# Kernel tuning notes

Hardware: AMD Instinct MI355X
Metric: run time of the kernel (lower is better)

## Reference

```python
import jax, jax.numpy as jnp
import numpy as np

IN_F = 4096
OUT_F = 4096
NNZ = 167772  # int(IN_F*OUT_F*0.01)
B, S = 4, 2048
ALPHA = 1.0  # self.alpha (privacy enabled)


def setup_inputs() -> dict:
    key = jax.random.key(0)
    k1, k2, k3, k4, k5 = jax.random.split(key, 5)
    x = jax.random.normal(k1, (B, S, IN_F), dtype=jnp.float32)
    # quantized-then-dequantized base weights stored in fp16
    base_weights = (jax.random.normal(k2, (OUT_F, IN_F), dtype=jnp.float32) * 0.02).astype(jnp.float16)
    # sparse outlier residual in COO form (equivalent to the module's CSR buffers)
    ortho_rows = jax.random.randint(k3, (NNZ,), 0, OUT_F, dtype=jnp.int32)
    ortho_cols = jax.random.randint(k4, (NNZ,), 0, IN_F, dtype=jnp.int32)
    ortho_vals = (jax.random.normal(k5, (NNZ,), dtype=jnp.float32) * 1e-3).astype(jnp.float16)
    return {"x": x, "base_weights": base_weights, "ortho_vals": ortho_vals,
            "ortho_rows": ortho_rows, "ortho_cols": ortho_cols}


def reference(x, base_weights, ortho_vals, ortho_rows, ortho_cols):
    orig_shape = x.shape
    orig_dtype = x.dtype
    x_flat = x.reshape(-1, IN_F)                                   # [N, in]
    # Base stream: fp16 GEMM, accumulated to fp32 (matches torch.mm on fp16 then .to(f32))
    out_base = jnp.matmul(x_flat.astype(jnp.float16), base_weights.T).astype(jnp.float32)  # [N, out]
    # Ortho stream: sparse CSR residual, computed in fp32 (vals upcast like the module)
    # Scatter the nnz outliers into a dense [out, in] matrix once, then a single GEMM
    # (same math as torch.sparse.mm over the CSR tensor, without per-chunk loops).
    w_ortho = jnp.zeros((OUT_F, IN_F), jnp.float32).at[ortho_rows, ortho_cols].add(
        ortho_vals.astype(jnp.float32))
    out_ortho = jnp.matmul(x_flat.astype(jnp.float32), w_ortho.T)  # [N, out]
    out_flat = out_base + ALPHA * out_ortho
    return out_flat.reshape(orig_shape[:-1] + (OUT_F,)).astype(orig_dtype)
```

## Files before the change

kernel.cpp:

```cpp
#include <hip/hip_runtime.h>
#include <stdint.h>

#define IN_F 4096
#define OUT_F 4096
#define NTOK 8192
#define NNZ_CNT 167772

typedef __attribute__((ext_vector_type(4))) float f32x4;
typedef __attribute__((ext_vector_type(8))) __bf16 bf16x8;
typedef __attribute__((ext_vector_type(8))) unsigned short u16x8;

__device__ __forceinline__ unsigned short f2bf(float f) {
  union { float f; unsigned int i; } u; u.f = f;
  unsigned int i = u.i;
  unsigned int r = (i + 0x7FFFu + ((i >> 16) & 1u)) >> 16;
  return (unsigned short)r;
}
__device__ __forceinline__ float bf2f(unsigned short h) {
  union { unsigned int i; float f; } u; u.i = ((unsigned int)h) << 16;
  return u.f;
}
__device__ __forceinline__ float sanitize(float f, float lim) {
  if (f >= -lim && f <= lim) return f;
  if (f > lim) return lim;
  if (f < -lim) return -lim;
  return 0.f;
}

__global__ void detect_dtype_kernel(const unsigned short* __restrict__ w, int* __restrict__ flag) {
  __shared__ int cnt;
  if (threadIdx.x == 0) cnt = 0;
  __syncthreads();
  int local = 0;
  for (int j = 0; j < 16; ++j) {
    unsigned short u = w[threadIdx.x * 16 + j];
    int e = (u >> 7) & 0xFF;
    if (u != 0 && e >= 107 && e <= 126) local++;
  }
  atomicAdd(&cnt, local);
  __syncthreads();
  if (threadIdx.x == 0) *flag = (cnt >= 3481) ? 0 : 1;
}

__global__ void prep_kernel(const float4* __restrict__ x, u16x8* __restrict__ xb, int n8x,
                            const void* __restrict__ bw, u16x8* __restrict__ wc, int n8w,
                            const int* __restrict__ flag) {
  const bool isf32 = (*flag != 0);
  const int stride = gridDim.x * blockDim.x;
  const int i0 = blockIdx.x * blockDim.x + threadIdx.x;
  for (int i = i0; i < n8x; i += stride) {
    float4 v0 = x[i * 2], v1 = x[i * 2 + 1];
    u16x8 o;
    o[0] = f2bf(sanitize(v0.x, 64.f)); o[1] = f2bf(sanitize(v0.y, 64.f));
    o[2] = f2bf(sanitize(v0.z, 64.f)); o[3] = f2bf(sanitize(v0.w, 64.f));
    o[4] = f2bf(sanitize(v1.x, 64.f)); o[5] = f2bf(sanitize(v1.y, 64.f));
    o[6] = f2bf(sanitize(v1.z, 64.f)); o[7] = f2bf(sanitize(v1.w, 64.f));
    xb[i] = o;
  }
  for (int i = i0; i < n8w; i += stride) {
    u16x8 o;
    if (isf32) {
      const float4* s = (const float4*)bw + i * 2;
      float4 v0 = s[0], v1 = s[1];
      o[0] = f2bf(sanitize(v0.x, 1.f)); o[1] = f2bf(sanitize(v0.y, 1.f));
      o[2] = f2bf(sanitize(v0.z, 1.f)); o[3] = f2bf(sanitize(v0.w, 1.f));
      o[4] = f2bf(sanitize(v1.x, 1.f)); o[5] = f2bf(sanitize(v1.y, 1.f));
      o[6] = f2bf(sanitize(v1.z, 1.f)); o[7] = f2bf(sanitize(v1.w, 1.f));
    } else {
      u16x8 v = ((const u16x8*)bw)[i];
#pragma unroll
      for (int j = 0; j < 8; ++j) o[j] = f2bf(sanitize(bf2f(v[j]), 1.f));
    }
    wc[i] = o;
  }
}

__global__ void scatter_kernel(const void* __restrict__ vals,
                               const int* __restrict__ rows,
                               const int* __restrict__ cols,
                               unsigned short* __restrict__ W,
                               const int* __restrict__ flag) {
  int i = blockIdx.x * blockDim.x + threadIdx.x;
  if (i >= NNZ_CNT) return;
  int r = rows[i], c = cols[i];
  if ((unsigned)r >= OUT_F || (unsigned)c >= IN_F) return;
  float v = (*flag != 0) ? ((const float*)vals)[i] : bf2f(((const unsigned short*)vals)[i]);
  v = sanitize(v, 1.f);
  unsigned int* addr = (unsigned int*)(W + (size_t)r * IN_F + (c & ~1));
  bool hi = (c & 1);
  unsigned int old = *addr, assumed;
  do {
    assumed = old;
    unsigned short h = hi ? (unsigned short)(assumed >> 16) : (unsigned short)(assumed & 0xFFFFu);
    unsigned short nh = f2bf(bf2f(h) + v);
    unsigned int nw = hi ? ((assumed & 0x0000FFFFu) | ((unsigned int)nh << 16))
                         : ((assumed & 0xFFFF0000u) | (unsigned int)nh);
    old = atomicCAS(addr, assumed, nw);
  } while (old != assumed);
}

#define GLOAD16(g, l)                                                                  \
  __builtin_amdgcn_global_load_lds((const __attribute__((address_space(1))) void*)(g), \
                                   (__attribute__((address_space(3))) void*)(l), 16, 0, 0)

__global__ __launch_bounds__(512, 2) void gemm256_kernel(
    const unsigned short* __restrict__ Abf,
    const unsigned short* __restrict__ Bw,
    float* __restrict__ C) {
  __shared__ __align__(16) char lds[131072];
  const int t = threadIdx.x;
  const int l = t & 63;
  const int wv = t >> 6;
  const int wm = wv >> 2;
  const int wn = wv & 3;
  const int l15 = l & 15;

  const int swz = (blockIdx.x & 7) * 64 + (blockIdx.x >> 3);
  const int bm = (swz >> 4) * 256;
  const int bn = (swz & 15) * 256;

  const int srow = t >> 2;
  const int sunit = (t & 3) ^ ((t >> 3) & 3);
  const unsigned short* aS0 = Abf + (size_t)(bm + srow) * IN_F + sunit * 8;
  const unsigned short* aS1 = aS0 + (size_t)128 * IN_F;
  const unsigned short* bS0 = Bw + (size_t)(bn + srow) * IN_F + sunit * 8;
  const unsigned short* bS1 = bS0 + (size_t)128 * IN_F;
  char* dstA = (char*)lds + wv * 1024;
  char* dstB = (char*)lds + 32768 + wv * 1024;

  const int u = (l >> 4) ^ ((l15 >> 1) & 3);
  const int iA = (wm * 128 + l15) * 4 + u;
  const int iB = 2048 + (wn * 64 + l15) * 4 + u;
  const bf16x8* smp = (const bf16x8*)lds;

  f32x4 acc[8][4] = {};

  GLOAD16(aS0 + 0, dstA + 0);          GLOAD16(aS1 + 0, dstA + 8192);
  GLOAD16(bS0 + 0, dstB + 0);          GLOAD16(bS1 + 0, dstB + 8192);
  GLOAD16(aS0 + 32, dstA + 16384);     GLOAD16(aS1 + 32, dstA + 16384 + 8192);
  GLOAD16(bS0 + 32, dstB + 16384);     GLOAD16(bS1 + 32, dstB + 16384 + 8192);
  GLOAD16(aS0 + 64, dstA + 65536);     GLOAD16(aS1 + 64, dstA + 65536 + 8192);
  GLOAD16(bS0 + 64, dstB + 65536);     GLOAD16(bS1 + 64, dstB + 65536 + 8192);
  asm volatile("s_waitcnt vmcnt(8)" ::: "memory");
  asm volatile("s_barrier" ::: "memory");

  for (int kt = 0; kt < 64; ++kt) {
    const int c = kt & 1;
    const int cU = c << 12;
    const int s1 = ((kt + 1 < 64) ? (kt + 1) : 63) * 64 + 32;
    const int s2 = ((kt + 2 < 64) ? (kt + 2) : 63) * 64;
    const int d1 = (c ^ 1) * 65536 + 16384;
    const int d2 = c * 65536;
    bf16x8 av[4], bv[4];

#pragma unroll
    for (int mi = 0; mi < 4; ++mi) av[mi] = smp[cU + iA + mi * 64];
#pragma unroll
    for (int ni = 0; ni < 4; ++ni) bv[ni] = smp[cU + iB + ni * 64];
    GLOAD16(aS0 + s1, dstA + d1);
    GLOAD16(aS1 + s1, dstA + d1 + 8192);
    asm volatile("s_barrier" ::: "memory");
    asm volatile("s_waitcnt lgkmcnt(0)" ::: "memory");
    __builtin_amdgcn_s_setprio(1);
#pragma unroll
    for (int mi = 0; mi < 4; ++mi)
#pragma unroll
      for (int ni = 0; ni < 4; ++ni)
        acc[mi][ni] = __builtin_amdgcn_mfma_f32_16x16x32_bf16(av[mi], bv[ni], acc[mi][ni], 0, 0, 0);
    __builtin_amdgcn_s_setprio(0);
    asm volatile("s_barrier" ::: "memory");

#pragma unroll
    for (int mi = 0; mi < 4; ++mi) av[mi] = smp[cU + iA + (mi + 4) * 64];
    GLOAD16(bS0 + s1, dstB + d1);
    GLOAD16(bS1 + s1, dstB + d1 + 8192);
    asm volatile("s_barrier" ::: "memory");
    asm volatile("s_waitcnt lgkmcnt(0)" ::: "memory");
    __builtin_amdgcn_s_setprio(1);
#pragma unroll
    for (int mi = 0; mi < 4; ++mi)
#pragma unroll
      for (int ni = 0; ni < 4; ++ni)
        acc[mi + 4][ni] = __builtin_amdgcn_mfma_f32_16x16x32_bf16(av[mi], bv[ni], acc[mi + 4][ni], 0, 0, 0);
    __builtin_amdgcn_s_setprio(0);
    asm volatile("s_waitcnt vmcnt(8)" ::: "memory");
    asm volatile("s_barrier" ::: "memory");

#pragma unroll
    for (int mi = 0; mi < 4; ++mi) av[mi] = smp[cU + 1024 + iA + mi * 64];
#pragma unroll
    for (int ni = 0; ni < 4; ++ni) bv[ni] = smp[cU + 1024 + iB + ni * 64];
    GLOAD16(aS0 + s2, dstA + d2);
    GLOAD16(aS1 + s2, dstA + d2 + 8192);
    asm volatile("s_barrier" ::: "memory");
    asm volatile("s_waitcnt lgkmcnt(0)" ::: "memory");
    __builtin_amdgcn_s_setprio(1);
#pragma unroll
    for (int mi = 0; mi < 4; ++mi)
#pragma unroll
      for (int ni = 0; ni < 4; ++ni)
        acc[mi][ni] = __builtin_amdgcn_mfma_f32_16x16x32_bf16(av[mi], bv[ni], acc[mi][ni], 0, 0, 0);
    __builtin_amdgcn_s_setprio(0);
    asm volatile("s_barrier" ::: "memory");

#pragma unroll
    for (int mi = 0; mi < 4; ++mi) av[mi] = smp[cU + 1024 + iA + (mi + 4) * 64];
    GLOAD16(bS0 + s2, dstB + d2);
    GLOAD16(bS1 + s2, dstB + d2 + 8192);
    asm volatile("s_barrier" ::: "memory");
    asm volatile("s_waitcnt lgkmcnt(0)" ::: "memory");
    __builtin_amdgcn_s_setprio(1);
#pragma unroll
    for (int mi = 0; mi < 4; ++mi)
#pragma unroll
      for (int ni = 0; ni < 4; ++ni)
        acc[mi + 4][ni] = __builtin_amdgcn_mfma_f32_16x16x32_bf16(av[mi], bv[ni], acc[mi + 4][ni], 0, 0, 0);
    __builtin_amdgcn_s_setprio(0);
    asm volatile("s_waitcnt vmcnt(8)" ::: "memory");
    asm volatile("s_barrier" ::: "memory");
  }

#pragma unroll
  for (int mi = 0; mi < 8; ++mi) {
#pragma unroll
    for (int ni = 0; ni < 4; ++ni) {
      int row0 = bm + wm * 128 + mi * 16 + ((l >> 4) << 2);
      int col = bn + wn * 64 + ni * 16 + l15;
#pragma unroll
      for (int r = 0; r < 4; ++r)
        C[(size_t)(row0 + r) * OUT_F + col] = acc[mi][ni][r];
    }
  }
}

__global__ __launch_bounds__(256, 3) void gemm_kernel(
    const float* __restrict__ Af, const unsigned short* __restrict__ Bw, float* __restrict__ C) {
  __shared__ bf16x8 smem[2048];
  const int tid = threadIdx.x;
  const int lane = tid & 63;
  const int wv = tid >> 6;
  const int bm = blockIdx.x * 128;
  const int bn = blockIdx.y * 128;
  const int srow = wv * 8 + (lane >> 3);
  const int scol = (lane & 7) * 8;
  const int wr = wv >> 1, wc = wv & 1;
  f32x4 acc[4][4] = {};
  const float* afp[4];
  const unsigned short* bptr[4];
#pragma unroll
  for (int q = 0; q < 4; ++q) {
    afp[q] = Af + (size_t)(bm + q * 32 + srow) * IN_F + scol;
    bptr[q] = Bw + (size_t)(bn + q * 32 + srow) * IN_F + scol;
  }
  char* smbase = (char*)smem;
  for (int k0 = 0; k0 < IN_F; k0 += 64) {
    __syncthreads();
#pragma unroll
    for (int q = 0; q < 4; ++q)
      GLOAD16(bptr[q] + k0, smbase + 16384 + q * 4096 + wv * 1024);
#pragma unroll
    for (int q = 0; q < 4; ++q) {
      const float* s = afp[q] + k0;
      float4 v0 = ((const float4*)s)[0];
      float4 v1 = ((const float4*)s)[1];
      u16x8 p;
      p[0] = f2bf(sanitize(v0.x, 64.f)); p[1] = f2bf(sanitize(v0.y, 64.f));
      p[2] = f2bf(sanitize(v0.z, 64.f)); p[3] = f2bf(sanitize(v0.w, 64.f));
      p[4] = f2bf(sanitize(v1.x, 64.f)); p[5] = f2bf(sanitize(v1.y, 64.f));
      p[6] = f2bf(sanitize(v1.z, 64.f)); p[7] = f2bf(sanitize(v1.w, 64.f));
      ((u16x8*)smem)[q * 256 + wv * 64 + lane] = p;
    }
    __syncthreads();
#pragma unroll
    for (int kk = 0; kk < 2; ++kk) {
      bf16x8 av[4], bv[4];
#pragma unroll
      for (int m = 0; m < 4; ++m)
        av[m] = smem[(wr * 64 + m * 16 + (lane & 15)) * 8 + kk * 4 + (lane >> 4)];
#pragma unroll
      for (int n = 0; n < 4; ++n)
        bv[n] = smem[1024 + (wc * 64 + n * 16 + (lane & 15)) * 8 + kk * 4 + (lane >> 4)];
#pragma unroll
      for (int m = 0; m < 4; ++m)
#pragma unroll
        for (int n = 0; n < 4; ++n)
          acc[m][n] = __builtin_amdgcn_mfma_f32_16x16x32_bf16(av[m], bv[n], acc[m][n], 0, 0, 0);
    }
  }
#pragma unroll
  for (int m = 0; m < 4; ++m)
#pragma unroll
    for (int n = 0; n < 4; ++n) {
      int row0 = bm + wr * 64 + m * 16 + ((lane >> 4) << 2);
      int col = bn + wc * 64 + n * 16 + (lane & 15);
#pragma unroll
      for (int r = 0; r < 4; ++r)
        C[(size_t)(row0 + r) * OUT_F + col] = acc[m][n][r];
    }
}

__global__ void naive_gemm_kernel(const float* __restrict__ x, const void* __restrict__ W,
                                  float* __restrict__ out, const int* __restrict__ flag) {
  const bool isf32 = (*flag != 0);
  int o = blockIdx.x * 256 + threadIdx.x;
  int t = blockIdx.y;
  const float* xr = x + (size_t)t * IN_F;
  float acc = 0.f;
  if (isf32) {
    const float* wr = (const float*)W + (size_t)o * IN_F;
    for (int k = 0; k < IN_F; ++k) acc += bf2f(f2bf(xr[k])) * bf2f(f2bf(sanitize(wr[k], 1.f)));
  } else {
    const unsigned short* wr = (const unsigned short*)W + (size_t)o * IN_F;
    for (int k = 0; k < IN_F; ++k) acc += bf2f(f2bf(xr[k])) * sanitize(bf2f(wr[k]), 1.f);
  }
  out[(size_t)t * OUT_F + o] = acc;
}
__global__ void naive_sparse_kernel(const float* __restrict__ x, const void* __restrict__ vals,
                                    const int* __restrict__ rows, const int* __restrict__ cols,
                                    float* __restrict__ out, const int* __restrict__ flag) {
  const bool isf32 = (*flag != 0);
  int t = blockIdx.x * 256 + threadIdx.x;
  if (t >= NTOK) return;
  const float* xr = x + (size_t)t * IN_F;
  float* orow = out + (size_t)t * OUT_F;
  for (int i = 0; i < NNZ_CNT; ++i) {
    int r = rows[i], c = cols[i];
    if ((unsigned)r >= OUT_F || (unsigned)c >= IN_F) continue;
    float v = isf32 ? ((const float*)vals)[i] : bf2f(((const unsigned short*)vals)[i]);
    orow[r] += sanitize(v, 1.f) * xr[c];
  }
}

extern "C" void kernel_launch(void* const* d_in, const int* in_sizes, int n_in,
                              void* d_out, int out_size, void* d_ws, size_t ws_size,
                              hipStream_t stream) {
  (void)out_size;
  const int NX = NTOK * IN_F, NW = OUT_F * IN_F;
  int ix = -1, ib = -1, qs[3], nq = 0;
  for (int i = 0; i < n_in; ++i) {
    if (in_sizes[i] == NX) ix = i;
    else if (in_sizes[i] == NW) ib = i;
    else if (in_sizes[i] == NNZ_CNT && nq < 3) qs[nq++] = i;
  }
  if (ix < 0 || ib < 0 || nq < 3) { ix = 0; ib = 1; qs[0] = 2; qs[1] = 3; qs[2] = 4; }
  const float* x = (const float*)d_in[ix];
  const void* bw = d_in[ib];
  const int* rows = (const int*)d_in[qs[1]];
  const void* vals;
  const int* cols;
  if (ix < ib) { vals = d_in[qs[0]]; cols = (const int*)d_in[qs[2]]; }
  else         { vals = d_in[qs[2]]; cols = (const int*)d_in[qs[0]]; }
  float* out = (float*)d_out;

  const size_t w_bytes = (size_t)OUT_F * IN_F * 2;
  const size_t xb_bytes = (size_t)NTOK * IN_F * 2;

  if (ws_size < w_bytes + 64) {
    int* flag = (int*)d_ws;
    hipLaunchKernelGGL(detect_dtype_kernel, dim3(1), dim3(256), 0, stream,
                       (const unsigned short*)bw, flag);
    hipLaunchKernelGGL(naive_gemm_kernel, dim3(OUT_F / 256, NTOK), dim3(256), 0, stream,
                       x, bw, out, flag);
    hipLaunchKernelGGL(naive_sparse_kernel, dim3((NTOK + 255) / 256), dim3(256), 0, stream,
                       x, vals, rows, cols, out, flag);
    return;
  }

  unsigned short* wcmb = (unsigned short*)d_ws;
  const bool big = ws_size >= w_bytes + xb_bytes + 4096;
  unsigned short* xb = (unsigned short*)((char*)d_ws + w_bytes);
  int* flag = (int*)((char*)d_ws + (big ? (w_bytes + xb_bytes) : w_bytes));

  hipLaunchKernelGGL(detect_dtype_kernel, dim3(1), dim3(256), 0, stream,
                     (const unsigned short*)bw, flag);
  hipLaunchKernelGGL(prep_kernel, dim3(4096), dim3(256), 0, stream,
                     (const float4*)x, (u16x8*)xb, big ? (NX / 8) : 0,
                     bw, (u16x8*)wcmb, NW / 8, flag);
  hipLaunchKernelGGL(scatter_kernel, dim3((NNZ_CNT + 255) / 256), dim3(256), 0, stream,
                     vals, rows, cols, wcmb, flag);

  if (big) {
    hipLaunchKernelGGL(gemm256_kernel, dim3((NTOK / 256) * (OUT_F / 256)), dim3(512), 0, stream,
                       xb, wcmb, out);
  } else {
    hipLaunchKernelGGL(gemm_kernel, dim3(NTOK / 128, OUT_F / 128), dim3(256), 0, stream,
                       x, wcmb, out);
  }
}
```

Baseline: 310.9 us.

## Fold dtype detection into kernels and cut GEMM main-loop barriers

Drops the separate single-block dtype-detection launch. Each prep, scatter and naive kernel block now probes the weight bytes itself through a shared-memory counter, which removes a launch and a dependent flag read from global memory. In the 256x256 GEMM main loop, the per-phase barrier plus lgkmcnt pairs are replaced by just two vmcnt-plus-barrier points per iteration, leaving LDS read waits to the compiler and cutting sync stalls between MFMA phases. The prep grid is also halved. The risks are redundant detection work in every block and possible LDS read/write races if the remaining barriers do not fully protect buffer reuse.

```diff
diff --git a/kernel.cpp b/kernel.cpp
--- a/kernel.cpp
+++ b/kernel.cpp
@@ -27,25 +27,26 @@
   return 0.f;
 }
 
-__global__ void detect_dtype_kernel(const unsigned short* __restrict__ w, int* __restrict__ flag) {
-  __shared__ int cnt;
-  if (threadIdx.x == 0) cnt = 0;
+__device__ __forceinline__ bool detect_isf32(const unsigned short* w, int tid, int* sh_cnt) {
+  if (tid == 0) *sh_cnt = 0;
   __syncthreads();
   int local = 0;
-  for (int j = 0; j < 16; ++j) {
-    unsigned short u = w[threadIdx.x * 16 + j];
-    int e = (u >> 7) & 0xFF;
-    if (u != 0 && e >= 107 && e <= 126) local++;
-  }
-  atomicAdd(&cnt, local);
+  if (tid < 256) {
+    for (int j = 0; j < 16; ++j) {
+      unsigned short u = w[tid * 16 + j];
+      int e = (u >> 7) & 0xFF;
+      if (u != 0 && e >= 107 && e <= 126) local++;
+    }
+  }
+  atomicAdd(sh_cnt, local);
   __syncthreads();
-  if (threadIdx.x == 0) *flag = (cnt >= 3481) ? 0 : 1;
+  return *sh_cnt < 3481;
 }
 
 __global__ void prep_kernel(const float4* __restrict__ x, u16x8* __restrict__ xb, int n8x,
-                            const void* __restrict__ bw, u16x8* __restrict__ wc, int n8w,
-                            const int* __restrict__ flag) {
-  const bool isf32 = (*flag != 0);
+                            const void* __restrict__ bw, u16x8* __restrict__ wc, int n8w) {
+  __shared__ int sh_cnt;
+  const bool isf32 = detect_isf32((const unsigned short*)bw, threadIdx.x, &sh_cnt);
   const int stride = gridDim.x * blockDim.x;
   const int i0 = blockIdx.x * blockDim.x + threadIdx.x;
   for (int i = i0; i < n8x; i += stride) {
@@ -79,12 +80,14 @@
                                const int* __restrict__ rows,
                                const int* __restrict__ cols,
                                unsigned short* __restrict__ W,
-                               const int* __restrict__ flag) {
+                               const void* __restrict__ bw_probe) {
+  __shared__ int sh_cnt;
+  const bool isf32 = detect_isf32((const unsigned short*)bw_probe, threadIdx.x, &sh_cnt);
   int i = blockIdx.x * blockDim.x + threadIdx.x;
   if (i >= NNZ_CNT) return;
   int r = rows[i], c = cols[i];
   if ((unsigned)r >= OUT_F || (unsigned)c >= IN_F) return;
-  float v = (*flag != 0) ? ((const float*)vals)[i] : bf2f(((const unsigned short*)vals)[i]);
+  float v = isf32 ? ((const float*)vals)[i] : bf2f(((const unsigned short*)vals)[i]);
   v = sanitize(v, 1.f);
   unsigned int* addr = (unsigned int*)(W + (size_t)r * IN_F + (c & ~1));
   bool hi = (c & 1);
@@ -141,8 +144,6 @@
   GLOAD16(bS0 + 32, dstB + 16384);     GLOAD16(bS1 + 32, dstB + 16384 + 8192);
   GLOAD16(aS0 + 64, dstA + 65536);     GLOAD16(aS1 + 64, dstA + 65536 + 8192);
   GLOAD16(bS0 + 64, dstB + 65536);     GLOAD16(bS1 + 64, dstB + 65536 + 8192);
-  asm volatile("s_waitcnt vmcnt(8)" ::: "memory");
-  asm volatile("s_barrier" ::: "memory");
 
   for (int kt = 0; kt < 64; ++kt) {
     const int c = kt & 1;
@@ -153,14 +154,14 @@
     const int d2 = c * 65536;
     bf16x8 av[4], bv[4];
 
+    asm volatile("s_waitcnt vmcnt(8)" ::: "memory");
+    asm volatile("s_barrier" ::: "memory");
 #pragma unroll
     for (int mi = 0; mi < 4; ++mi) av[mi] = smp[cU + iA + mi * 64];
 #pragma unroll
     for (int ni = 0; ni < 4; ++ni) bv[ni] = smp[cU + iB + ni * 64];
     GLOAD16(aS0 + s1, dstA + d1);
     GLOAD16(aS1 + s1, dstA + d1 + 8192);
-    asm volatile("s_barrier" ::: "memory");
-    asm volatile("s_waitcnt lgkmcnt(0)" ::: "memory");
     __builtin_amdgcn_s_setprio(1);
 #pragma unroll
     for (int mi = 0; mi < 4; ++mi)
@@ -168,14 +169,10 @@
       for (int ni = 0; ni < 4; ++ni)
         acc[mi][ni] = __builtin_amdgcn_mfma_f32_16x16x32_bf16(av[mi], bv[ni], acc[mi][ni], 0, 0, 0);
     __builtin_amdgcn_s_setprio(0);
-    asm volatile("s_barrier" ::: "memory");
-
 #pragma unroll
     for (int mi = 0; mi < 4; ++mi) av[mi] = smp[cU + iA + (mi + 4) * 64];
     GLOAD16(bS0 + s1, dstB + d1);
     GLOAD16(bS1 + s1, dstB + d1 + 8192);
-    asm volatile("s_barrier" ::: "memory");
-    asm volatile("s_waitcnt lgkmcnt(0)" ::: "memory");
     __builtin_amdgcn_s_setprio(1);
 #pragma unroll
     for (int mi = 0; mi < 4; ++mi)
@@ -183,17 +180,15 @@
       for (int ni = 0; ni < 4; ++ni)
         acc[mi + 4][ni] = __builtin_amdgcn_mfma_f32_16x16x32_bf16(av[mi], bv[ni], acc[mi + 4][ni], 0, 0, 0);
     __builtin_amdgcn_s_setprio(0);
+
     asm volatile("s_waitcnt vmcnt(8)" ::: "memory");
     asm volatile("s_barrier" ::: "memory");
-
 #pragma unroll
     for (int mi = 0; mi < 4; ++mi) av[mi] = smp[cU + 1024 + iA + mi * 64];
 #pragma unroll
     for (int ni = 0; ni < 4; ++ni) bv[ni] = smp[cU + 1024 + iB + ni * 64];
     GLOAD16(aS0 + s2, dstA + d2);
     GLOAD16(aS1 + s2, dstA + d2 + 8192);
-    asm volatile("s_barrier" ::: "memory");
-    asm volatile("s_waitcnt lgkmcnt(0)" ::: "memory");
     __builtin_amdgcn_s_setprio(1);
 #pragma unroll
     for (int mi = 0; mi < 4; ++mi)
@@ -201,14 +196,10 @@
       for (int ni = 0; ni < 4; ++ni)
         acc[mi][ni] = __builtin_amdgcn_mfma_f32_16x16x32_bf16(av[mi], bv[ni], acc[mi][ni], 0, 0, 0);
     __builtin_amdgcn_s_setprio(0);
-    asm volatile("s_barrier" ::: "memory");
-
 #pragma unroll
     for (int mi = 0; mi < 4; ++mi) av[mi] = smp[cU + 1024 + iA + (mi + 4) * 64];
     GLOAD16(bS0 + s2, dstB + d2);
     GLOAD16(bS1 + s2, dstB + d2 + 8192);
-    asm volatile("s_barrier" ::: "memory");
-    asm volatile("s_waitcnt lgkmcnt(0)" ::: "memory");
     __builtin_amdgcn_s_setprio(1);
 #pragma unroll
     for (int mi = 0; mi < 4; ++mi)
@@ -216,8 +207,6 @@
       for (int ni = 0; ni < 4; ++ni)
         acc[mi + 4][ni] = __builtin_amdgcn_mfma_f32_16x16x32_bf16(av[mi], bv[ni], acc[mi + 4][ni], 0, 0, 0);
     __builtin_amdgcn_s_setprio(0);
-    asm volatile("s_waitcnt vmcnt(8)" ::: "memory");
-    asm volatile("s_barrier" ::: "memory");
   }
 
 #pragma unroll
@@ -300,8 +289,9 @@
 }
 
 __global__ void naive_gemm_kernel(const float* __restrict__ x, const void* __restrict__ W,
-                                  float* __restrict__ out, const int* __restrict__ flag) {
-  const bool isf32 = (*flag != 0);
+                                  float* __restrict__ out) {
+  __shared__ int sh_cnt;
+  const bool isf32 = detect_isf32((const unsigned short*)W, threadIdx.x, &sh_cnt);
   int o = blockIdx.x * 256 + threadIdx.x;
   int t = blockIdx.y;
   const float* xr = x + (size_t)t * IN_F;
@@ -317,8 +307,9 @@
 }
 __global__ void naive_sparse_kernel(const float* __restrict__ x, const void* __restrict__ vals,
                                     const int* __restrict__ rows, const int* __restrict__ cols,
-                                    float* __restrict__ out, const int* __restrict__ flag) {
-  const bool isf32 = (*flag != 0);
+                                    float* __restrict__ out, const void* __restrict__ bw_probe) {
+  __shared__ int sh_cnt;
+  const bool isf32 = detect_isf32((const unsigned short*)bw_probe, threadIdx.x, &sh_cnt);
   int t = blockIdx.x * 256 + threadIdx.x;
   if (t >= NTOK) return;
   const float* xr = x + (size_t)t * IN_F;
@@ -356,28 +347,22 @@
   const size_t xb_bytes = (size_t)NTOK * IN_F * 2;
 
   if (ws_size < w_bytes + 64) {
-    int* flag = (int*)d_ws;
-    hipLaunchKernelGGL(detect_dtype_kernel, dim3(1), dim3(256), 0, stream,
-                       (const unsigned short*)bw, flag);
     hipLaunchKernelGGL(naive_gemm_kernel, dim3(OUT_F / 256, NTOK), dim3(256), 0, stream,
-                       x, bw, out, flag);
+                       x, bw, out);
     hipLaunchKernelGGL(naive_sparse_kernel, dim3((NTOK + 255) / 256), dim3(256), 0, stream,
-                       x, vals, rows, cols, out, flag);
+                       x, vals, rows, cols, out, bw);
     return;
   }
 
   unsigned short* wcmb = (unsigned short*)d_ws;
-  const bool big = ws_size >= w_bytes + xb_bytes + 4096;
+  const bool big = ws_size >= w_bytes + xb_bytes;
   unsigned short* xb = (unsigned short*)((char*)d_ws + w_bytes);
-  int* flag = (int*)((char*)d_ws + (big ? (w_bytes + xb_bytes) : w_bytes));
-
-  hipLaunchKernelGGL(detect_dtype_kernel, dim3(1), dim3(256), 0, stream,
-                     (const unsigned short*)bw, flag);
-  hipLaunchKernelGGL(prep_kernel, dim3(4096), dim3(256), 0, stream,
+
+  hipLaunchKernelGGL(prep_kernel, dim3(2048), dim3(256), 0, stream,
                      (const float4*)x, (u16x8*)xb, big ? (NX / 8) : 0,
-                     bw, (u16x8*)wcmb, NW / 8, flag);
+                     bw, (u16x8*)wcmb, NW / 8);
   hipLaunchKernelGGL(scatter_kernel, dim3((NNZ_CNT + 255) / 256), dim3(256), 0, stream,
-                     vals, rows, cols, wcmb, flag);
+                     vals, rows, cols, wcmb, bw);
 
   if (big) {
     hipLaunchKernelGGL(gemm256_kernel, dim3((NTOK / 256) * (OUT_F / 256)), dim3(512), 0, stream,
```

Measured after the change: 305.2 us (median of 2 runs). Within noise of the previous version (-1.8%).
